# Kernel tuning notes

Hardware: AMD Instinct MI355X
Metric: run time of the kernel (lower is better)

Reference implementation:

```python
import jax, jax.numpy as jnp
import numpy as np

B, N, D, H, FF = 2, 2048, 768, 12, 3072
HD = D // H
RADIUS = 2.0
COORD_DIM = 3
LN_EPS = 1e-5


def _layernorm(x, g, b):
    m = jnp.mean(x, axis=-1, keepdims=True)
    v = jnp.mean((x - m) ** 2, axis=-1, keepdims=True)
    return (x - m) * jax.lax.rsqrt(v + LN_EPS) * g + b


def setup_inputs() -> dict:
    key = jax.random.key(0)
    ks = jax.random.split(key, 16)
    s = 0.02
    return {
        "x": jax.random.normal(ks[0], (B, N, D), jnp.float32),
        "coords": jax.random.uniform(ks[1], (B, N, COORD_DIM), jnp.float32) * 10.0,
        "w_qkv": jax.random.normal(ks[2], (D, 3 * D), jnp.float32) * s,
        "b_qkv": jnp.zeros((3 * D,), jnp.float32),
        "w_out": jax.random.normal(ks[3], (D, D), jnp.float32) * s,
        "b_out": jnp.zeros((D,), jnp.float32),
        "w_ff1": jax.random.normal(ks[4], (D, FF), jnp.float32) * s,
        "b_ff1": jnp.zeros((FF,), jnp.float32),
        "w_ff2": jax.random.normal(ks[5], (FF, D), jnp.float32) * s,
        "b_ff2": jnp.zeros((D,), jnp.float32),
        "g1": jnp.ones((D,), jnp.float32),
        "beta1": jnp.zeros((D,), jnp.float32),
        "g2": jnp.ones((D,), jnp.float32),
        "beta2": jnp.zeros((D,), jnp.float32),
    }


def reference(x, coords, w_qkv, b_qkv, w_out, b_out, w_ff1, b_ff1,
              w_ff2, b_ff2, g1, beta1, g2, beta2):
    # --- attention sub-block ---
    residual = x
    xn = _layernorm(x, g1, beta1)
    qkv = xn @ w_qkv + b_qkv                       # [B,N,3D]
    qkv = qkv.reshape(B, N, 3, H, HD)
    q, k, v = qkv[:, :, 0], qkv[:, :, 1], qkv[:, :, 2]   # [B,N,H,HD]

    # geometric radius mask: attend only to tokens within Euclidean RADIUS
    d2 = jnp.sum((coords[:, :, None, :] - coords[:, None, :, :]) ** 2, axis=-1)  # [B,N,N]
    mask = d2 <= RADIUS * RADIUS                   # self-distance 0 -> always true

    scores = jnp.einsum("bqhd,bkhd->bhqk", q, k) / jnp.sqrt(jnp.float32(HD))
    scores = jnp.where(mask[:, None, :, :], scores, jnp.float32(-1e9))
    attn = jax.nn.softmax(scores, axis=-1)
    attn_out = jnp.einsum("bhqk,bkhd->bqhd", attn, v).reshape(B, N, D)
    attn_out = attn_out @ w_out + b_out            # dropout=0 (eval)
    x = residual + attn_out

    # --- FFN sub-block ---
    residual = x
    xn = _layernorm(x, g2, beta2)
    h = jax.nn.gelu(xn @ w_ff1 + b_ff1, approximate=False)
    ff_out = h @ w_ff2 + b_ff2
    return residual + ff_out
```

## Files before the change

kernel.cpp:

```cpp
#include <hip/hip_runtime.h>
#include <hip/hip_bf16.h>

typedef unsigned short ushort_t;
typedef __attribute__((ext_vector_type(4))) float f32x4;
typedef __attribute__((ext_vector_type(8))) short s16x8;

#define DEV static __device__ __forceinline__

constexpr int Bb = 2, Nn = 2048, Dd = 768, Hh = 12, FFf = 3072;
constexpr int MTOK = Bb * Nn;
constexpr int QKVN = 3 * Dd;

DEV unsigned short f2bf(float f) {
    union { float f; unsigned int i; } x; x.f = f;
    unsigned int r = x.i + 0x7FFFu + ((x.i >> 16) & 1u);
    return (unsigned short)(r >> 16);
}

DEV void gload16(const void* g, void* l) {
    __builtin_amdgcn_global_load_lds(
        (const __attribute__((address_space(1))) void*)g,
        (__attribute__((address_space(3))) void*)l, 16, 0, 0);
}

DEV int xcd_swz(int lin, int n) {
    return (lin & 7) * (n >> 3) + (lin >> 3);
}

DEV float gelu_fast(float x) {
    float u = x * (0.7978845608f + 0.0356774081f * x * x);
    float e = __builtin_amdgcn_exp2f(2.885390082f * u);
    float th = 1.f - 2.f / (e + 1.f);
    return 0.5f * x * (1.f + th);
}

__global__ void k_transpose_all(const float* __restrict__ w_qkv, const float* __restrict__ w_out,
                                const float* __restrict__ w_ff1, const float* __restrict__ w_ff2,
                                unsigned short* __restrict__ o_qkv, unsigned short* __restrict__ o_out,
                                unsigned short* __restrict__ o_ff1, unsigned short* __restrict__ o_ff2) {
    __shared__ float t[32][33];
    int id = blockIdx.x;
    const float* in; unsigned short* out; int K, N, tid;
    if (id < 1728)      { in = w_qkv; out = o_qkv; K = 768;  N = 2304; tid = id; }
    else if (id < 2304) { in = w_out; out = o_out; K = 768;  N = 768;  tid = id - 1728; }
    else if (id < 4608) { in = w_ff1; out = o_ff1; K = 768;  N = 3072; tid = id - 2304; }
    else                { in = w_ff2; out = o_ff2; K = 3072; N = 768;  tid = id - 4608; }
    int nbx = N >> 5;
    int bx = (tid % nbx) * 32, by = (tid / nbx) * 32;
    int tx = threadIdx.x, ty = threadIdx.y;
#pragma unroll
    for (int i = 0; i < 4; i++)
        t[ty + 8 * i][tx] = in[(size_t)(by + ty + 8 * i) * N + bx + tx];
    __syncthreads();
#pragma unroll
    for (int i = 0; i < 4; i++)
        out[(size_t)(bx + ty + 8 * i) * K + by + tx] = f2bf(t[tx][ty + 8 * i]);
}

DEV int cell3(float x, float y, float z) {
    int cx = (int)(x * 0.5f); cx = cx > 4 ? 4 : cx;
    int cy = (int)(y * 0.5f); cy = cy > 4 ? 4 : cy;
    int cz = (int)(z * 0.5f); cz = cz > 4 ? 4 : cz;
    return (cz * 5 + cy) * 5 + cx;
}

__global__ __launch_bounds__(256) void k_sort(const float* __restrict__ coords,
                                              int* __restrict__ s2o,
                                              float4* __restrict__ c4s) {
    int b = blockIdx.y;
    int i = blockIdx.x * 4 + (threadIdx.x >> 6);
    int lane = threadIdx.x & 63;
    const float* cb = coords + (size_t)b * Nn * 3;
    float cix = cb[3 * i], ciy = cb[3 * i + 1], ciz = cb[3 * i + 2];
    int celli = cell3(cix, ciy, ciz);
    int pos = 0;
    for (int it = 0; it < Nn / 64; it++) {
        int j = it * 64 + lane;
        int cj = cell3(cb[3 * j], cb[3 * j + 1], cb[3 * j + 2]);
        bool before = (cj < celli) || (cj == celli && j < i);
        pos += __popcll(__ballot(before));
    }
    if (lane == 0) {
        s2o[b * Nn + pos] = i;
        c4s[b * Nn + pos] = make_float4(cix, ciy, ciz, 0.f);
    }
}

__global__ __launch_bounds__(256) void k_mask(const float4* __restrict__ c4s,
                                              unsigned long long* __restrict__ mb) {
    int qt = blockIdx.x, ks = blockIdx.y, b = blockIdx.z;
    __shared__ float4 ck[256];
    int t = threadIdx.x;
    ck[t] = c4s[b * Nn + ks * 256 + t];
    __syncthreads();
    int r = t >> 2, c = t & 3;
    int q = qt * 64 + r;
    float4 cq = c4s[b * Nn + q];
    unsigned long long w = 0;
#pragma unroll 8
    for (int j = 0; j < 64; j++) {
        float4 k4 = ck[c * 64 + j];
        float dx = __fsub_rn(cq.x, k4.x);
        float dy = __fsub_rn(cq.y, k4.y);
        float dz = __fsub_rn(cq.z, k4.z);
        float d2 = __fadd_rn(__fadd_rn(__fmul_rn(dx, dx), __fmul_rn(dy, dy)),
                             __fmul_rn(dz, dz));
        if (d2 <= 4.0f) w |= 1ull << j;
    }
    mb[((size_t)(b * Nn + q) << 5) + ks * 4 + c] = w;
}

__global__ __launch_bounds__(64) void k_tiles(const unsigned long long* __restrict__ mb,
                                              int* __restrict__ tl) {
    int q64 = blockIdx.x, b = blockIdx.y;
    int lane = threadIdx.x;
    unsigned long long v = 0;
    if (lane < 32) {
        const unsigned long long* base = mb + ((size_t)(b * Nn + q64 * 64) << 5) + lane;
        for (int r = 0; r < 64; r++) v |= base[(size_t)r << 5];
    }
    unsigned long long nz = __ballot(v != 0);
    int idx = __popcll(nz & ((1ull << lane) - 1));
    int* o = tl + (b * 32 + q64) * 33;
    if (v != 0) o[1 + idx] = lane;
    if (lane == 0) o[0] = __popcll(nz);
}

__global__ __launch_bounds__(128) void k_gatherK(const unsigned short* __restrict__ qkv,
                                                 const int* __restrict__ s2o,
                                                 unsigned short* __restrict__ Ksort) {
    int ns = blockIdx.x & (Nn - 1);
    int b = blockIdx.x >> 11;
    int t = threadIdx.x;
    int orig = s2o[b * Nn + ns];
    const s16x8* src = (const s16x8*)(qkv + ((size_t)b * Nn + orig) * QKVN + Dd);
    s16x8* dst = (s16x8*)(Ksort + ((size_t)b * Nn + ns) * Dd);
    if (t < 96) dst[t] = src[t];
}

__global__ __launch_bounds__(256) void k_vt(const unsigned short* __restrict__ qkv,
                                            const int* __restrict__ s2o,
                                            unsigned short* __restrict__ VtT) {
    __shared__ unsigned short Ld[64][72];
    int ns0 = blockIdx.x * 64;
    int bh = blockIdx.y;
    int b = bh / Hh, h = bh % Hh;
    int t = threadIdx.x;
#pragma unroll
    for (int i = 0; i < 2; i++) {
        int item = t + 256 * i;
        int row = item >> 3, ch = (item & 7) * 8;
        int orig = s2o[b * Nn + ns0 + row];
        *(s16x8*)&Ld[row][ch] =
            *(const s16x8*)(qkv + ((size_t)b * Nn + orig) * QKVN + 2 * Dd + h * 64 + ch);
    }
    __syncthreads();
    int vd = (t >> 5) * 8, vkp = (t & 31) * 2;
#pragma unroll
    for (int j = 0; j < 8; j++) {
        unsigned int pack = (unsigned int)Ld[vkp][vd + j] |
                            ((unsigned int)Ld[vkp + 1][vd + j] << 16);
        *(unsigned int*)((char*)VtT +
                         (((size_t)bh * 64 + vd + j) * Nn + ns0 + vkp) * 2) = pack;
    }
}

DEV float wred_sum(float v) {
#pragma unroll
    for (int o = 32; o; o >>= 1) v += __shfl_down(v, o, 64);
    return v;
}

__global__ __launch_bounds__(256) void k_ln(const float* __restrict__ x,
                                            const float* __restrict__ g,
                                            const float* __restrict__ be,
                                            unsigned short* __restrict__ out) {
    int row = blockIdx.x;
    const float* xr = x + (size_t)row * Dd;
    int t = threadIdx.x;
    float v0 = xr[t], v1 = xr[t + 256], v2 = xr[t + 512];
    float s = v0 + v1 + v2;
    float sq = v0 * v0 + v1 * v1 + v2 * v2;
    __shared__ float r1[4], r2[4];
    float ws = wred_sum(s), wq = wred_sum(sq);
    int wid = t >> 6, lane = t & 63;
    if (lane == 0) { r1[wid] = ws; r2[wid] = wq; }
    __syncthreads();
    s = r1[0] + r1[1] + r1[2] + r1[3];
    sq = r2[0] + r2[1] + r2[2] + r2[3];
    float mean = s * (1.f / Dd);
    float var = sq * (1.f / Dd) - mean * mean;
    float rs = rsqrtf(var + 1e-5f);
    unsigned short* orow = out + (size_t)row * Dd;
    orow[t]       = f2bf((v0 - mean) * rs * g[t]       + be[t]);
    orow[t + 256] = f2bf((v1 - mean) * rs * g[t + 256] + be[t + 256]);
    orow[t + 512] = f2bf((v2 - mean) * rs * g[t + 512] + be[t + 512]);
}

template <int EPI>
__global__ __launch_bounds__(512, 2) void k_gemm256(const unsigned short* __restrict__ A,
                                                    const unsigned short* __restrict__ Bt,
                                                    const float* __restrict__ bias,
                                                    unsigned short* __restrict__ outp,
                                                    int M, int N, int K) {
    constexpr int BM = 256, BN = 256, BK = 32;
    __shared__ unsigned short As[3][BM * BK];
    __shared__ unsigned short Bs[3][BN * BK];
    int NB = N >> 8;
    int id = xcd_swz(blockIdx.x, gridDim.x);
    int m0 = (id / NB) * BM, n0 = (id % NB) * BN;
    int t = threadIdx.x;
    int wid = t >> 6, lane = t & 63;
    int wr = wid >> 2, wc = wid & 3;
    int lg = lane >> 4, lr = lane & 15;
    f32x4 acc[8][4] = {};

    int srow = t >> 2, sch = t & 3;
    auto stage = [&](int buf, int kt) {
        int k0 = kt * BK;
#pragma unroll
        for (int g = 0; g < 2; g++) {
            int ar = g * 128 + srow;
            gload16(A + (size_t)(m0 + ar) * K + k0 + ((sch ^ (ar & 3)) * 8),
                    (char*)As[buf] + g * 8192 + wid * 1024);
        }
#pragma unroll
        for (int g = 0; g < 2; g++) {
            int br = g * 128 + srow;
            gload16(Bt + (size_t)(n0 + br) * K + k0 + ((sch ^ (br & 3)) * 8),
                    (char*)Bs[buf] + g * 8192 + wid * 1024);
        }
    };

    int NT = K / BK;
    stage(0, 0);
    stage(1, 1);
    for (int k = 0; k < NT; k++) {
        int cur = k % 3;
        if (k + 1 < NT) {
            asm volatile("s_waitcnt vmcnt(4)" ::: "memory");
        } else {
            asm volatile("s_waitcnt vmcnt(0)" ::: "memory");
        }
        __builtin_amdgcn_sched_barrier(0);
        __builtin_amdgcn_s_barrier();
        __builtin_amdgcn_sched_barrier(0);
        if (k + 2 < NT) stage((k + 2) % 3, k + 2);
        s16x8 af[8], bfr[4];
#pragma unroll
        for (int i = 0; i < 8; i++) {
            int row = wr * 128 + i * 16 + lr;
            af[i] = *(const s16x8*)((const char*)As[cur] + row * 64 + ((lg ^ (row & 3)) << 4));
        }
#pragma unroll
        for (int j = 0; j < 4; j++) {
            int row = wc * 64 + j * 16 + lr;
            bfr[j] = *(const s16x8*)((const char*)Bs[cur] + row * 64 + ((lg ^ (row & 3)) << 4));
        }
#pragma unroll
        for (int i = 0; i < 8; i++)
#pragma unroll
            for (int j = 0; j < 4; j++)
                acc[i][j] = __builtin_amdgcn_mfma_f32_16x16x32_bf16(
                    af[i], bfr[j], acc[i][j], 0, 0, 0);
    }

    int mrow = m0 + wr * 128;
    int ncol = n0 + wc * 64;
#pragma unroll
    for (int i = 0; i < 8; i++) {
#pragma unroll
        for (int j = 0; j < 4; j++) {
            int nn = ncol + j * 16 + lr;
            float bs = bias[nn];
#pragma unroll
            for (int r = 0; r < 4; r++) {
                int mm = mrow + i * 16 + lg * 4 + r;
                float v = acc[i][j][r] + bs;
                if (EPI == 1) v = gelu_fast(v);
                outp[(size_t)mm * N + nn] = f2bf(v);
            }
        }
    }
}

#define GEMM_PIPE_LOOP(NT)                                                              \
    stage(0, 0);                                                                        \
    if ((NT) > 1) stage(1, 1);                                                          \
    for (int t = 0; t < (NT); t++) {                                                    \
        int cur = t % 3;                                                                \
        if (t + 2 < (NT)) {                                                             \
            stage((t + 2) % 3, t + 2);                                                  \
            asm volatile("s_waitcnt vmcnt(8)" ::: "memory");                            \
        } else if (t + 1 < (NT)) {                                                      \
            asm volatile("s_waitcnt vmcnt(4)" ::: "memory");                            \
        } else {                                                                        \
            asm volatile("s_waitcnt vmcnt(0)" ::: "memory");                            \
        }                                                                               \
        __builtin_amdgcn_sched_barrier(0);                                              \
        __builtin_amdgcn_s_barrier();                                                   \
        const unsigned short* Ab = As[cur];                                             \
        const unsigned short* Bbp = Bs[cur];                                            \
        s16x8 af[4], bfr[4];                                                            \
        _Pragma("unroll")                                                               \
        for (int i = 0; i < 4; i++) {                                                   \
            af[i]  = *(const s16x8*)&Ab[(wr * 64 + i * 16 + lr) * 32 + lg * 8];         \
            bfr[i] = *(const s16x8*)&Bbp[(wc * 64 + i * 16 + lr) * 32 + lg * 8];        \
        }                                                                               \
        _Pragma("unroll")                                                               \
        for (int mi = 0; mi < 4; mi++)                                                  \
            _Pragma("unroll")                                                           \
            for (int ni = 0; ni < 4; ni++)                                              \
                acc[mi][ni] = __builtin_amdgcn_mfma_f32_16x16x32_bf16(                  \
                    af[mi], bfr[ni], acc[mi][ni], 0, 0, 0);                             \
        __builtin_amdgcn_s_barrier();                                                   \
    }

template <int SPLIT>
__global__ __launch_bounds__(256) void k_gemm_sk(const unsigned short* __restrict__ A,
                                                 const unsigned short* __restrict__ Bt,
                                                 float* __restrict__ part,
                                                 int M, int N, int K) {
    constexpr int BM = 128, BN = 128, BK = 32;
    __shared__ unsigned short As[3][BM * BK];
    __shared__ unsigned short Bs[3][BN * BK];
    int NB = N >> 7, MB = M >> 7;
    int id = xcd_swz(blockIdx.x, gridDim.x);
    int nb = id % NB;
    int mbk = (id / NB) % MB;
    int kz = id / (NB * MB);
    int m0 = mbk * BM, n0 = nb * BN;
    int Kc = K / SPLIT, kb = kz * (Kc / BK);
    int t = threadIdx.x;
    int wid = t >> 6, lane = t & 63;
    int wr = wid >> 1, wc = wid & 1;
    int lg = lane >> 4, lr = lane & 15;
    f32x4 acc[4][4] = {};

    int srow = wid * 32 + (lane >> 2);
    int scol = (lane & 3) * 8;
    const unsigned short* Ag = A + (size_t)(m0 + srow) * K + scol;
    const unsigned short* Bg = Bt + (size_t)(n0 + srow) * K + scol;

    auto stage = [&](int buf, int kt) {
        int k0 = (kb + kt) * BK;
        char* Al = (char*)As[buf] + wid * 2048;
        char* Bl = (char*)Bs[buf] + wid * 2048;
        gload16(Ag + k0, Al);
        gload16(Ag + k0 + (size_t)16 * K, Al + 1024);
        gload16(Bg + k0, Bl);
        gload16(Bg + k0 + (size_t)16 * K, Bl + 1024);
    };
    int nt = Kc / BK;
    GEMM_PIPE_LOOP(nt)

    float* po = part + (size_t)kz * M * N;
    int mrow = m0 + wr * 64;
    int ncol = n0 + wc * 64;
#pragma unroll
    for (int mi = 0; mi < 4; mi++)
#pragma unroll
        for (int ni = 0; ni < 4; ni++) {
            int nn = ncol + ni * 16 + lr;
#pragma unroll
            for (int r = 0; r < 4; r++) {
                int mm = mrow + mi * 16 + lg * 4 + r;
                po[(size_t)mm * N + nn] = acc[mi][ni][r];
            }
        }
}

__global__ __launch_bounds__(256) void k_reduce4_ln(const float* __restrict__ part,
                                                    const float* __restrict__ bias,
                                                    const float* __restrict__ res,
                                                    const float* __restrict__ g,
                                                    const float* __restrict__ be,
                                                    float* __restrict__ x2,
                                                    unsigned short* __restrict__ xn,
                                                    int MN) {
    int wid = threadIdx.x >> 6, lane = threadIdx.x & 63;
    int row = blockIdx.x * 4 + wid;
    size_t base = (size_t)row * Dd;
    f32x4 v[3];
    float s = 0.f, sq = 0.f;
#pragma unroll
    for (int j = 0; j < 3; j++) {
        int col = j * 256 + lane * 4;
        f32x4 a0 = *(const f32x4*)(part + base + col);
        f32x4 a1 = *(const f32x4*)(part + (size_t)MN + base + col);
        f32x4 a2 = *(const f32x4*)(part + 2 * (size_t)MN + base + col);
        f32x4 a3 = *(const f32x4*)(part + 3 * (size_t)MN + base + col);
        f32x4 r = *(const f32x4*)(res + base + col);
        f32x4 bs = *(const f32x4*)(bias + col);
#pragma unroll
        for (int q = 0; q < 4; q++) {
            v[j][q] = (a0[q] + a1[q]) + (a2[q] + a3[q]) + bs[q] + r[q];
            s += v[j][q];
            sq += v[j][q] * v[j][q];
        }
        *(f32x4*)(x2 + base + col) = v[j];
    }
    s = wred_sum(s); sq = wred_sum(sq);
    s = __shfl(s, 0, 64); sq = __shfl(sq, 0, 64);
    float mean = s * (1.f / Dd);
    float var = sq * (1.f / Dd) - mean * mean;
    float rs = rsqrtf(var + 1e-5f);
#pragma unroll
    for (int j = 0; j < 3; j++) {
        int col = j * 256 + lane * 4;
        f32x4 gg = *(const f32x4*)(g + col);
        f32x4 bb = *(const f32x4*)(be + col);
        ushort4 o;
        o.x = f2bf((v[j][0] - mean) * rs * gg[0] + bb[0]);
        o.y = f2bf((v[j][1] - mean) * rs * gg[1] + bb[1]);
        o.z = f2bf((v[j][2] - mean) * rs * gg[2] + bb[2]);
        o.w = f2bf((v[j][3] - mean) * rs * gg[3] + bb[3]);
        *(ushort4*)(xn + base + col) = o;
    }
}

__global__ __launch_bounds__(256) void k_reduce4(const float* __restrict__ part,
                                                 const float* __restrict__ bias,
                                                 const float* __restrict__ res,
                                                 float* __restrict__ out,
                                                 int MN, int N) {
    int i = (blockIdx.x * 256 + threadIdx.x) * 4;
    f32x4 a0 = *(const f32x4*)(part + i);
    f32x4 a1 = *(const f32x4*)(part + (size_t)MN + i);
    f32x4 a2 = *(const f32x4*)(part + 2 * (size_t)MN + i);
    f32x4 a3 = *(const f32x4*)(part + 3 * (size_t)MN + i);
    f32x4 r = *(const f32x4*)(res + i);
    f32x4 bs = *(const f32x4*)(bias + (i % N));
    f32x4 o;
#pragma unroll
    for (int j = 0; j < 4; j++) o[j] = (a0[j] + a1[j]) + (a2[j] + a3[j]) + bs[j] + r[j];
    *(f32x4*)(out + i) = o;
}

constexpr float SC2 = 0.125f * 1.44269504088896340736f;
constexpr float PMASK = -3.0e38f;
constexpr float MINIT = -1.0e30f;

__global__ __launch_bounds__(256) void k_attn(const unsigned short* __restrict__ qkv,
                                              const unsigned short* __restrict__ Ksort,
                                              const unsigned short* __restrict__ VtT,
                                              const int* __restrict__ s2o,
                                              const uint2* __restrict__ mb,
                                              const int* __restrict__ tl,
                                              unsigned short* __restrict__ out) {
    int lin = blockIdx.x;
    int id = (lin & 7) * 96 + (lin >> 3);
    int q64 = id & 31;
    int hb = id >> 5;
    int h = hb % Hh, b = hb / Hh;
    int bh = b * Hh + h;

    __shared__ __align__(16) char sm[2 * 16384 + 4 * 2048];

    int t = threadIdx.x, wid = t >> 6, lane = t & 63;
    int lg = lane >> 4, lr = lane & 15;
    int sw = lr & 7;
    int qbase = q64 * 64 + wid * 16;

    int oq = s2o[b * Nn + qbase + lr];
    const unsigned short* Qb = qkv + ((size_t)b * Nn + oq) * QKVN + h * 64;
    s16x8 qf0 = *(const s16x8*)(Qb + lg * 8);
    s16x8 qf1 = *(const s16x8*)(Qb + 32 + lg * 8);

    const uint2* mrow = mb + ((size_t)(b * Nn + qbase + lr) << 5);
    const int* tle = tl + (b * 32 + q64) * 33;
    int tlv = (lane < 33) ? tle[lane] : 0;
    int cnt = __shfl(tlv, 0, 64);

    int srow = lane >> 3, sch = lane & 7;
    int krow = wid * 8 + srow;
    int kx = sch ^ (krow & 7);
    const unsigned short* Kg0 = Ksort + ((size_t)b * Nn + krow) * Dd + h * 64 + kx * 8;
    const unsigned short* Vg0 = VtT + ((size_t)bh * 64 + krow) * Nn + kx * 8;
    char* pw = sm + 32768 + wid * 2048 + lr * 128;

    float m2 = MINIT, l_run = 0.f;
    f32x4 oacc[4] = {};

    int tid0 = __shfl(tlv, 1, 64);
    uint2 Mw = mrow[tid0];
    {
        char* Kl = sm + wid * 1024;
        gload16(Kg0 + (size_t)(tid0 * 64) * Dd, Kl);
        gload16(Kg0 + (size_t)(tid0 * 64 + 32) * Dd, Kl + 4096);
        char* Vl = sm + 8192 + wid * 1024;
        gload16(Vg0 + tid0 * 64, Vl);
        gload16(Vg0 + tid0 * 64 + 32 * (size_t)Nn, Vl + 4096);
    }
    __syncthreads();

    for (int ti = 0; ti < cnt; ti++) {
        int cur = ti & 1;
        uint2 MwN;
        if (ti + 1 < cnt) {
            int tidn = __shfl(tlv, 2 + ti, 64);
            char* Kl = sm + (cur ^ 1) * 16384 + wid * 1024;
            gload16(Kg0 + (size_t)(tidn * 64) * Dd, Kl);
            gload16(Kg0 + (size_t)(tidn * 64 + 32) * Dd, Kl + 4096);
            char* Vl = sm + (cur ^ 1) * 16384 + 8192 + wid * 1024;
            gload16(Vg0 + tidn * 64, Vl);
            gload16(Vg0 + tidn * 64 + 32 * (size_t)Nn, Vl + 4096);
            MwN = mrow[tidn];
        }

        if (__any((Mw.x | Mw.y) != 0)) {
            const char* Kbuf = sm + cur * 16384;
            const char* Vbuf = Kbuf + 8192;

            __builtin_amdgcn_s_setprio(1);
            f32x4 st[4];
#pragma unroll
            for (int s = 0; s < 4; s++) {
                const char* kr = Kbuf + (s * 16 + lr) * 128;
                s16x8 kf0 = *(const s16x8*)(kr + ((lg ^ sw) << 4));
                s16x8 kf1 = *(const s16x8*)(kr + (((4 + lg) ^ sw) << 4));
                f32x4 z = {};
                z = __builtin_amdgcn_mfma_f32_16x16x32_bf16(kf0, qf0, z, 0, 0, 0);
                st[s] = __builtin_amdgcn_mfma_f32_16x16x32_bf16(kf1, qf1, z, 0, 0, 0);
            }
            __builtin_amdgcn_s_setprio(0);

            float p[4][4];
            float mt = PMASK;
#pragma unroll
            for (int s = 0; s < 4; s++) {
                unsigned int wsel = (s < 2) ? Mw.x : Mw.y;
#pragma unroll
                for (int r = 0; r < 4; r++) {
                    float sv = st[s][r] * SC2;
                    unsigned int bit = (wsel >> ((s & 1) * 16 + lg * 4 + r)) & 1u;
                    p[s][r] = bit ? sv : PMASK;
                    mt = fmaxf(mt, p[s][r]);
                }
            }
            mt = fmaxf(mt, __shfl_xor(mt, 16, 64));
            mt = fmaxf(mt, __shfl_xor(mt, 32, 64));

            if (!__all(mt <= m2 + 11.5416f)) {
                float mn2 = fmaxf(m2, mt);
                float fac = __builtin_amdgcn_exp2f(m2 - mn2);
                l_run *= fac;
                m2 = mn2;
                float fr[4];
#pragma unroll
                for (int r = 0; r < 4; r++) fr[r] = __shfl(fac, (lane & 48) + lg * 4 + r, 64);
#pragma unroll
                for (int dt = 0; dt < 4; dt++)
#pragma unroll
                    for (int r = 0; r < 4; r++) oacc[dt][r] *= fr[r];
            }

            float lt = 0.f;
#pragma unroll
            for (int s = 0; s < 4; s++)
#pragma unroll
                for (int r = 0; r < 4; r++) {
                    p[s][r] = __builtin_amdgcn_exp2f(p[s][r] - m2);
                    lt += p[s][r];
                }
            lt += __shfl_xor(lt, 16, 64);
            lt += __shfl_xor(lt, 32, 64);
            l_run += lt;

#pragma unroll
            for (int s = 0; s < 4; s++) {
                unsigned int lo = (unsigned int)f2bf(p[s][0]) | ((unsigned int)f2bf(p[s][1]) << 16);
                unsigned int hi = (unsigned int)f2bf(p[s][2]) | ((unsigned int)f2bf(p[s][3]) << 16);
                unsigned long long u = (unsigned long long)lo | ((unsigned long long)hi << 32);
                int chunk = (s * 2 + (lg >> 1)) ^ sw;
                *(unsigned long long*)(pw + (chunk << 4) + (lg & 1) * 8) = u;
            }

            __builtin_amdgcn_s_setprio(1);
#pragma unroll
            for (int c = 0; c < 2; c++) {
                s16x8 pf = *(const s16x8*)(pw + (((c * 4 + lg) ^ sw) << 4));
#pragma unroll
                for (int dt = 0; dt < 4; dt++) {
                    const char* vr = Vbuf + (dt * 16 + lr) * 128;
                    s16x8 vf = *(const s16x8*)(vr + (((c * 4 + lg) ^ sw) << 4));
                    oacc[dt] = __builtin_amdgcn_mfma_f32_16x16x32_bf16(pf, vf, oacc[dt], 0, 0, 0);
                }
            }
            __builtin_amdgcn_s_setprio(0);
        }

        __syncthreads();
        Mw = MwN;
    }

    float lr4[4];
    int orow[4];
#pragma unroll
    for (int r = 0; r < 4; r++) {
        lr4[r] = __shfl(l_run, (lane & 48) + lg * 4 + r, 64);
        orow[r] = s2o[b * Nn + qbase + lg * 4 + r];
    }
#pragma unroll
    for (int dt = 0; dt < 4; dt++)
#pragma unroll
        for (int r = 0; r < 4; r++) {
            float v = oacc[dt][r] / lr4[r];
            out[((size_t)b * Nn + orow[r]) * Dd + h * 64 + dt * 16 + lr] = f2bf(v);
        }
}

extern "C" void kernel_launch(void* const* d_in, const int* in_sizes, int n_in,
                              void* d_out, int out_size, void* d_ws, size_t ws_size,
                              hipStream_t stream) {
    const float* x      = (const float*)d_in[0];
    const float* coords = (const float*)d_in[1];
    const float* w_qkv  = (const float*)d_in[2];
    const float* b_qkv  = (const float*)d_in[3];
    const float* w_out  = (const float*)d_in[4];
    const float* b_out  = (const float*)d_in[5];
    const float* w_ff1  = (const float*)d_in[6];
    const float* b_ff1  = (const float*)d_in[7];
    const float* w_ff2  = (const float*)d_in[8];
    const float* b_ff2  = (const float*)d_in[9];
    const float* g1     = (const float*)d_in[10];
    const float* beta1  = (const float*)d_in[11];
    const float* g2     = (const float*)d_in[12];
    const float* beta2  = (const float*)d_in[13];

    char* ws = (char*)d_ws;
    size_t off = 0;
    auto alloc = [&](size_t bytes) {
        char* p = ws + off;
        off += (bytes + 255) & ~(size_t)255;
        return p;
    };
    unsigned short* w_qkv_t = (unsigned short*)alloc((size_t)QKVN * Dd * 2);
    unsigned short* w_out_t = (unsigned short*)alloc((size_t)Dd * Dd * 2);
    unsigned short* w_ff1_t = (unsigned short*)alloc((size_t)FFf * Dd * 2);
    unsigned short* w_ff2_t = (unsigned short*)alloc((size_t)Dd * FFf * 2);
    float4*         c4s     = (float4*)alloc((size_t)MTOK * 16);
    int*            s2o     = (int*)alloc((size_t)MTOK * 4);
    unsigned long long* mbits = (unsigned long long*)alloc((size_t)MTOK * 32 * 8);
    int*            tl      = (int*)alloc((size_t)Bb * 32 * 33 * 4);
    unsigned short* xn      = (unsigned short*)alloc((size_t)MTOK * Dd * 2);
    unsigned short* hbuf    = (unsigned short*)alloc((size_t)MTOK * FFf * 2);
    float*          x2      = (float*)alloc((size_t)MTOK * Dd * 4);
    unsigned short* attn_o  = (unsigned short*)alloc((size_t)MTOK * Dd * 2);
    unsigned short* qkv     = (unsigned short*)alloc((size_t)MTOK * QKVN * 2);
    unsigned short* Ksort   = (unsigned short*)alloc((size_t)MTOK * Dd * 2);
    unsigned short* VtT     = (unsigned short*)alloc((size_t)Bb * Hh * 64 * Nn * 2);
    float*          partial = (float*)alloc((size_t)4 * MTOK * Dd * 4);

    k_transpose_all<<<dim3(6912), dim3(32, 8), 0, stream>>>(
        w_qkv, w_out, w_ff1, w_ff2, w_qkv_t, w_out_t, w_ff1_t, w_ff2_t);
    k_sort<<<dim3(Nn / 4, Bb), 256, 0, stream>>>(coords, s2o, c4s);
    k_mask<<<dim3(Nn / 64, 8, Bb), 256, 0, stream>>>(c4s, mbits);
    k_tiles<<<dim3(32, Bb), 64, 0, stream>>>(mbits, tl);

    k_ln<<<MTOK, 256, 0, stream>>>(x, g1, beta1, xn);
    k_gemm256<0><<<dim3((MTOK / 256) * (QKVN / 256)), 512, 0, stream>>>(
        xn, w_qkv_t, b_qkv, qkv, MTOK, QKVN, Dd);
    k_gatherK<<<dim3(MTOK), 128, 0, stream>>>(qkv, s2o, Ksort);
    k_vt<<<dim3(Nn / 64, Bb * Hh), 256, 0, stream>>>(qkv, s2o, VtT);
    k_attn<<<dim3((Nn / 64) * Hh * Bb), 256, 0, stream>>>(
        qkv, Ksort, VtT, s2o, (const uint2*)mbits, tl, attn_o);
    k_gemm_sk<4><<<dim3((Dd / 128) * (MTOK / 128) * 4), 256, 0, stream>>>(
        attn_o, w_out_t, partial, MTOK, Dd, Dd);
    k_reduce4_ln<<<dim3(MTOK / 4), 256, 0, stream>>>(
        partial, b_out, x, g2, beta2, x2, xn, MTOK * Dd);
    k_gemm256<1><<<dim3((MTOK / 256) * (FFf / 256)), 512, 0, stream>>>(
        xn, w_ff1_t, b_ff1, hbuf, MTOK, FFf, Dd);
    k_gemm_sk<4><<<dim3((Dd / 128) * (MTOK / 128) * 4), 256, 0, stream>>>(
        hbuf, w_ff2_t, partial, MTOK, Dd, FFf);
    k_reduce4<<<dim3(MTOK * Dd / 1024), 256, 0, stream>>>(
        partial, b_ff2, x2, (float*)d_out, MTOK * Dd, Dd);
}
```

Before: 226.6 us.

## Run the whole block in spatially sorted token order and swap the GEMM tile

The first layernorm now gathers tokens into sorted order, so QKV, attention, the projections and the FFN all run on sorted rows. The final reduce scatters results back to the original positions. This removes the separate K gather kernel, the Ksort buffer and the indirect loads in k_vt and k_attn. The 256x256 BK32 triple-buffered GEMM for QKV and FF1 is also replaced by a 128x128 BK64 double-buffered kernel, which gives more blocks but less reuse per block.

```diff
diff --git a/kernel.cpp b/kernel.cpp
--- a/kernel.cpp
+++ b/kernel.cpp
@@ -126,20 +126,7 @@
     if (lane == 0) o[0] = __popcll(nz);
 }
 
-__global__ __launch_bounds__(128) void k_gatherK(const unsigned short* __restrict__ qkv,
-                                                 const int* __restrict__ s2o,
-                                                 unsigned short* __restrict__ Ksort) {
-    int ns = blockIdx.x & (Nn - 1);
-    int b = blockIdx.x >> 11;
-    int t = threadIdx.x;
-    int orig = s2o[b * Nn + ns];
-    const s16x8* src = (const s16x8*)(qkv + ((size_t)b * Nn + orig) * QKVN + Dd);
-    s16x8* dst = (s16x8*)(Ksort + ((size_t)b * Nn + ns) * Dd);
-    if (t < 96) dst[t] = src[t];
-}
-
 __global__ __launch_bounds__(256) void k_vt(const unsigned short* __restrict__ qkv,
-                                            const int* __restrict__ s2o,
                                             unsigned short* __restrict__ VtT) {
     __shared__ unsigned short Ld[64][72];
     int ns0 = blockIdx.x * 64;
@@ -150,9 +137,8 @@
     for (int i = 0; i < 2; i++) {
         int item = t + 256 * i;
         int row = item >> 3, ch = (item & 7) * 8;
-        int orig = s2o[b * Nn + ns0 + row];
         *(s16x8*)&Ld[row][ch] =
-            *(const s16x8*)(qkv + ((size_t)b * Nn + orig) * QKVN + 2 * Dd + h * 64 + ch);
+            *(const s16x8*)(qkv + ((size_t)b * Nn + ns0 + row) * QKVN + 2 * Dd + h * 64 + ch);
     }
     __syncthreads();
     int vd = (t >> 5) * 8, vkp = (t & 31) * 2;
@@ -171,12 +157,14 @@
     return v;
 }
 
-__global__ __launch_bounds__(256) void k_ln(const float* __restrict__ x,
-                                            const float* __restrict__ g,
-                                            const float* __restrict__ be,
-                                            unsigned short* __restrict__ out) {
+__global__ __launch_bounds__(256) void k_ln_g(const float* __restrict__ x,
+                                              const int* __restrict__ s2o,
+                                              const float* __restrict__ g,
+                                              const float* __restrict__ be,
+                                              unsigned short* __restrict__ out) {
     int row = blockIdx.x;
-    const float* xr = x + (size_t)row * Dd;
+    int orig = (row & ~(Nn - 1)) | s2o[row];
+    const float* xr = x + (size_t)orig * Dd;
     int t = threadIdx.x;
     float v0 = xr[t], v1 = xr[t + 256], v2 = xr[t + 512];
     float s = v0 + v1 + v2;
@@ -198,123 +186,98 @@
 }
 
 template <int EPI>
-__global__ __launch_bounds__(512, 2) void k_gemm256(const unsigned short* __restrict__ A,
-                                                    const unsigned short* __restrict__ Bt,
-                                                    const float* __restrict__ bias,
-                                                    unsigned short* __restrict__ outp,
-                                                    int M, int N, int K) {
-    constexpr int BM = 256, BN = 256, BK = 32;
-    __shared__ unsigned short As[3][BM * BK];
-    __shared__ unsigned short Bs[3][BN * BK];
-    int NB = N >> 8;
+__global__ __launch_bounds__(256) void k_gemm64(const unsigned short* __restrict__ A,
+                                                const unsigned short* __restrict__ Bt,
+                                                const float* __restrict__ bias,
+                                                unsigned short* __restrict__ outp,
+                                                int M, int N, int K) {
+    constexpr int BM = 128, BN = 128, BK = 64;
+    __shared__ unsigned short As[2][BM * BK];
+    __shared__ unsigned short Bs[2][BN * BK];
+    int NB = N >> 7;
     int id = xcd_swz(blockIdx.x, gridDim.x);
     int m0 = (id / NB) * BM, n0 = (id % NB) * BN;
     int t = threadIdx.x;
     int wid = t >> 6, lane = t & 63;
-    int wr = wid >> 2, wc = wid & 3;
+    int wr = wid >> 1, wc = wid & 1;
     int lg = lane >> 4, lr = lane & 15;
-    f32x4 acc[8][4] = {};
-
-    int srow = t >> 2, sch = t & 3;
+    int sw = lr & 7;
+    f32x4 acc[4][4] = {};
+
+    int srow = lane >> 3;
+    int sch = (lane & 7) ^ srow;
+    const unsigned short* Ag = A + (size_t)m0 * K + sch * 8;
+    const unsigned short* Bg = Bt + (size_t)n0 * K + sch * 8;
+
     auto stage = [&](int buf, int kt) {
         int k0 = kt * BK;
 #pragma unroll
-        for (int g = 0; g < 2; g++) {
-            int ar = g * 128 + srow;
-            gload16(A + (size_t)(m0 + ar) * K + k0 + ((sch ^ (ar & 3)) * 8),
-                    (char*)As[buf] + g * 8192 + wid * 1024);
-        }
-#pragma unroll
-        for (int g = 0; g < 2; g++) {
-            int br = g * 128 + srow;
-            gload16(Bt + (size_t)(n0 + br) * K + k0 + ((sch ^ (br & 3)) * 8),
-                    (char*)Bs[buf] + g * 8192 + wid * 1024);
+        for (int g = 0; g < 4; g++) {
+            int row = wid * 32 + g * 8 + srow;
+            gload16(Ag + (size_t)row * K + k0, (char*)As[buf] + (wid * 4 + g) * 1024);
+        }
+#pragma unroll
+        for (int g = 0; g < 4; g++) {
+            int row = wid * 32 + g * 8 + srow;
+            gload16(Bg + (size_t)row * K + k0, (char*)Bs[buf] + (wid * 4 + g) * 1024);
         }
     };
 
     int NT = K / BK;
     stage(0, 0);
-    stage(1, 1);
     for (int k = 0; k < NT; k++) {
-        int cur = k % 3;
+        int cur = k & 1;
         if (k + 1 < NT) {
-            asm volatile("s_waitcnt vmcnt(4)" ::: "memory");
+            stage(cur ^ 1, k + 1);
+            asm volatile("s_waitcnt vmcnt(8)" ::: "memory");
         } else {
             asm volatile("s_waitcnt vmcnt(0)" ::: "memory");
         }
         __builtin_amdgcn_sched_barrier(0);
         __builtin_amdgcn_s_barrier();
-        __builtin_amdgcn_sched_barrier(0);
-        if (k + 2 < NT) stage((k + 2) % 3, k + 2);
-        s16x8 af[8], bfr[4];
-#pragma unroll
-        for (int i = 0; i < 8; i++) {
-            int row = wr * 128 + i * 16 + lr;
-            af[i] = *(const s16x8*)((const char*)As[cur] + row * 64 + ((lg ^ (row & 3)) << 4));
-        }
-#pragma unroll
-        for (int j = 0; j < 4; j++) {
-            int row = wc * 64 + j * 16 + lr;
-            bfr[j] = *(const s16x8*)((const char*)Bs[cur] + row * 64 + ((lg ^ (row & 3)) << 4));
-        }
-#pragma unroll
-        for (int i = 0; i < 8; i++)
-#pragma unroll
-            for (int j = 0; j < 4; j++)
-                acc[i][j] = __builtin_amdgcn_mfma_f32_16x16x32_bf16(
-                    af[i], bfr[j], acc[i][j], 0, 0, 0);
-    }
-
-    int mrow = m0 + wr * 128;
+        const char* Ab = (const char*)As[cur];
+        const char* Bbp = (const char*)Bs[cur];
+#pragma unroll
+        for (int s = 0; s < 2; s++) {
+            s16x8 af[4], bfr[4];
+#pragma unroll
+            for (int i = 0; i < 4; i++) {
+                int row = wr * 64 + i * 16 + lr;
+                af[i] = *(const s16x8*)(Ab + row * 128 + (((s * 4 + lg) ^ sw) << 4));
+            }
+#pragma unroll
+            for (int j = 0; j < 4; j++) {
+                int row = wc * 64 + j * 16 + lr;
+                bfr[j] = *(const s16x8*)(Bbp + row * 128 + (((s * 4 + lg) ^ sw) << 4));
+            }
+#pragma unroll
+            for (int mi = 0; mi < 4; mi++)
+#pragma unroll
+                for (int ni = 0; ni < 4; ni++)
+                    acc[mi][ni] = __builtin_amdgcn_mfma_f32_16x16x32_bf16(
+                        af[mi], bfr[ni], acc[mi][ni], 0, 0, 0);
+        }
+        __builtin_amdgcn_s_barrier();
+    }
+
+    int mrow = m0 + wr * 64;
     int ncol = n0 + wc * 64;
 #pragma unroll
-    for (int i = 0; i < 8; i++) {
-#pragma unroll
-        for (int j = 0; j < 4; j++) {
-            int nn = ncol + j * 16 + lr;
+    for (int mi = 0; mi < 4; mi++) {
+#pragma unroll
+        for (int ni = 0; ni < 4; ni++) {
+            int nn = ncol + ni * 16 + lr;
             float bs = bias[nn];
 #pragma unroll
             for (int r = 0; r < 4; r++) {
-                int mm = mrow + i * 16 + lg * 4 + r;
-                float v = acc[i][j][r] + bs;
+                int mm = mrow + mi * 16 + lg * 4 + r;
+                float v = acc[mi][ni][r] + bs;
                 if (EPI == 1) v = gelu_fast(v);
                 outp[(size_t)mm * N + nn] = f2bf(v);
             }
         }
     }
 }
-
-#define GEMM_PIPE_LOOP(NT)                                                              \
-    stage(0, 0);                                                                        \
-    if ((NT) > 1) stage(1, 1);                                                          \
-    for (int t = 0; t < (NT); t++) {                                                    \
-        int cur = t % 3;                                                                \
-        if (t + 2 < (NT)) {                                                             \
-            stage((t + 2) % 3, t + 2);                                                  \
-            asm volatile("s_waitcnt vmcnt(8)" ::: "memory");                            \
-        } else if (t + 1 < (NT)) {                                                      \
-            asm volatile("s_waitcnt vmcnt(4)" ::: "memory");                            \
-        } else {                                                                        \
-            asm volatile("s_waitcnt vmcnt(0)" ::: "memory");                            \
-        }                                                                               \
-        __builtin_amdgcn_sched_barrier(0);                                              \
-        __builtin_amdgcn_s_barrier();                                                   \
-        const unsigned short* Ab = As[cur];                                             \
-        const unsigned short* Bbp = Bs[cur];                                            \
-        s16x8 af[4], bfr[4];                                                            \
-        _Pragma("unroll")                                                               \
-        for (int i = 0; i < 4; i++) {                                                   \
-            af[i]  = *(const s16x8*)&Ab[(wr * 64 + i * 16 + lr) * 32 + lg * 8];         \
-            bfr[i] = *(const s16x8*)&Bbp[(wc * 64 + i * 16 + lr) * 32 + lg * 8];        \
-        }                                                                               \
-        _Pragma("unroll")                                                               \
-        for (int mi = 0; mi < 4; mi++)                                                  \
-            _Pragma("unroll")                                                           \
-            for (int ni = 0; ni < 4; ni++)                                              \
-                acc[mi][ni] = __builtin_amdgcn_mfma_f32_16x16x32_bf16(                  \
-                    af[mi], bfr[ni], acc[mi][ni], 0, 0, 0);                             \
-        __builtin_amdgcn_s_barrier();                                                   \
-    }
 
 template <int SPLIT>
 __global__ __launch_bounds__(256) void k_gemm_sk(const unsigned short* __restrict__ A,
@@ -352,7 +315,36 @@
         gload16(Bg + k0 + (size_t)16 * K, Bl + 1024);
     };
     int nt = Kc / BK;
-    GEMM_PIPE_LOOP(nt)
+    stage(0, 0);
+    if (nt > 1) stage(1, 1);
+    for (int k = 0; k < nt; k++) {
+        int cur = k % 3;
+        if (k + 2 < nt) {
+            stage((k + 2) % 3, k + 2);
+            asm volatile("s_waitcnt vmcnt(8)" ::: "memory");
+        } else if (k + 1 < nt) {
+            asm volatile("s_waitcnt vmcnt(4)" ::: "memory");
+        } else {
+            asm volatile("s_waitcnt vmcnt(0)" ::: "memory");
+        }
+        __builtin_amdgcn_sched_barrier(0);
+        __builtin_amdgcn_s_barrier();
+        const unsigned short* Ab = As[cur];
+        const unsigned short* Bbp = Bs[cur];
+        s16x8 af[4], bfr[4];
+#pragma unroll
+        for (int i = 0; i < 4; i++) {
+            af[i]  = *(const s16x8*)&Ab[(wr * 64 + i * 16 + lr) * 32 + lg * 8];
+            bfr[i] = *(const s16x8*)&Bbp[(wc * 64 + i * 16 + lr) * 32 + lg * 8];
+        }
+#pragma unroll
+        for (int mi = 0; mi < 4; mi++)
+#pragma unroll
+            for (int ni = 0; ni < 4; ni++)
+                acc[mi][ni] = __builtin_amdgcn_mfma_f32_16x16x32_bf16(
+                    af[mi], bfr[ni], acc[mi][ni], 0, 0, 0);
+        __builtin_amdgcn_s_barrier();
+    }
 
     float* po = part + (size_t)kz * M * N;
     int mrow = m0 + wr * 64;
@@ -372,7 +364,8 @@
 
 __global__ __launch_bounds__(256) void k_reduce4_ln(const float* __restrict__ part,
                                                     const float* __restrict__ bias,
-                                                    const float* __restrict__ res,
+                                                    const float* __restrict__ x,
+                                                    const int* __restrict__ s2o,
                                                     const float* __restrict__ g,
                                                     const float* __restrict__ be,
                                                     float* __restrict__ x2,
@@ -380,7 +373,9 @@
                                                     int MN) {
     int wid = threadIdx.x >> 6, lane = threadIdx.x & 63;
     int row = blockIdx.x * 4 + wid;
+    int orig = (row & ~(Nn - 1)) | s2o[row];
     size_t base = (size_t)row * Dd;
+    size_t obase = (size_t)orig * Dd;
     f32x4 v[3];
     float s = 0.f, sq = 0.f;
 #pragma unroll
@@ -390,7 +385,7 @@
         f32x4 a1 = *(const f32x4*)(part + (size_t)MN + base + col);
         f32x4 a2 = *(const f32x4*)(part + 2 * (size_t)MN + base + col);
         f32x4 a3 = *(const f32x4*)(part + 3 * (size_t)MN + base + col);
-        f32x4 r = *(const f32x4*)(res + base + col);
+        f32x4 r = *(const f32x4*)(x + obase + col);
         f32x4 bs = *(const f32x4*)(bias + col);
 #pragma unroll
         for (int q = 0; q < 4; q++) {
@@ -419,22 +414,32 @@
     }
 }
 
-__global__ __launch_bounds__(256) void k_reduce4(const float* __restrict__ part,
-                                                 const float* __restrict__ bias,
-                                                 const float* __restrict__ res,
-                                                 float* __restrict__ out,
-                                                 int MN, int N) {
-    int i = (blockIdx.x * 256 + threadIdx.x) * 4;
-    f32x4 a0 = *(const f32x4*)(part + i);
-    f32x4 a1 = *(const f32x4*)(part + (size_t)MN + i);
-    f32x4 a2 = *(const f32x4*)(part + 2 * (size_t)MN + i);
-    f32x4 a3 = *(const f32x4*)(part + 3 * (size_t)MN + i);
-    f32x4 r = *(const f32x4*)(res + i);
-    f32x4 bs = *(const f32x4*)(bias + (i % N));
-    f32x4 o;
-#pragma unroll
-    for (int j = 0; j < 4; j++) o[j] = (a0[j] + a1[j]) + (a2[j] + a3[j]) + bs[j] + r[j];
-    *(f32x4*)(out + i) = o;
+__global__ __launch_bounds__(256) void k_reduce4_sc(const float* __restrict__ part,
+                                                    const float* __restrict__ bias,
+                                                    const float* __restrict__ res,
+                                                    const int* __restrict__ s2o,
+                                                    float* __restrict__ out,
+                                                    int MN) {
+    int wid = threadIdx.x >> 6, lane = threadIdx.x & 63;
+    int row = blockIdx.x * 4 + wid;
+    int orig = (row & ~(Nn - 1)) | s2o[row];
+    size_t base = (size_t)row * Dd;
+    size_t obase = (size_t)orig * Dd;
+#pragma unroll
+    for (int j = 0; j < 3; j++) {
+        int col = j * 256 + lane * 4;
+        f32x4 a0 = *(const f32x4*)(part + base + col);
+        f32x4 a1 = *(const f32x4*)(part + (size_t)MN + base + col);
+        f32x4 a2 = *(const f32x4*)(part + 2 * (size_t)MN + base + col);
+        f32x4 a3 = *(const f32x4*)(part + 3 * (size_t)MN + base + col);
+        f32x4 r = *(const f32x4*)(res + base + col);
+        f32x4 bs = *(const f32x4*)(bias + col);
+        f32x4 o;
+#pragma unroll
+        for (int q = 0; q < 4; q++)
+            o[q] = (a0[q] + a1[q]) + (a2[q] + a3[q]) + bs[q] + r[q];
+        *(f32x4*)(out + obase + col) = o;
+    }
 }
 
 constexpr float SC2 = 0.125f * 1.44269504088896340736f;
@@ -442,9 +447,7 @@
 constexpr float MINIT = -1.0e30f;
 
 __global__ __launch_bounds__(256) void k_attn(const unsigned short* __restrict__ qkv,
-                                              const unsigned short* __restrict__ Ksort,
                                               const unsigned short* __restrict__ VtT,
-                                              const int* __restrict__ s2o,
                                               const uint2* __restrict__ mb,
                                               const int* __restrict__ tl,
                                               unsigned short* __restrict__ out) {
@@ -462,8 +465,7 @@
     int sw = lr & 7;
     int qbase = q64 * 64 + wid * 16;
 
-    int oq = s2o[b * Nn + qbase + lr];
-    const unsigned short* Qb = qkv + ((size_t)b * Nn + oq) * QKVN + h * 64;
+    const unsigned short* Qb = qkv + ((size_t)b * Nn + qbase + lr) * QKVN + h * 64;
     s16x8 qf0 = *(const s16x8*)(Qb + lg * 8);
     s16x8 qf1 = *(const s16x8*)(Qb + 32 + lg * 8);
 
@@ -475,7 +477,7 @@
     int srow = lane >> 3, sch = lane & 7;
     int krow = wid * 8 + srow;
     int kx = sch ^ (krow & 7);
-    const unsigned short* Kg0 = Ksort + ((size_t)b * Nn + krow) * Dd + h * 64 + kx * 8;
+    const unsigned short* Kg0 = qkv + ((size_t)b * Nn + krow) * QKVN + Dd + h * 64 + kx * 8;
     const unsigned short* Vg0 = VtT + ((size_t)bh * 64 + krow) * Nn + kx * 8;
     char* pw = sm + 32768 + wid * 2048 + lr * 128;
 
@@ -486,8 +488,8 @@
     uint2 Mw = mrow[tid0];
     {
         char* Kl = sm + wid * 1024;
-        gload16(Kg0 + (size_t)(tid0 * 64) * Dd, Kl);
-        gload16(Kg0 + (size_t)(tid0 * 64 + 32) * Dd, Kl + 4096);
+        gload16(Kg0 + (size_t)(tid0 * 64) * QKVN, Kl);
+        gload16(Kg0 + (size_t)(tid0 * 64 + 32) * QKVN, Kl + 4096);
         char* Vl = sm + 8192 + wid * 1024;
         gload16(Vg0 + tid0 * 64, Vl);
         gload16(Vg0 + tid0 * 64 + 32 * (size_t)Nn, Vl + 4096);
@@ -500,8 +502,8 @@
         if (ti + 1 < cnt) {
             int tidn = __shfl(tlv, 2 + ti, 64);
             char* Kl = sm + (cur ^ 1) * 16384 + wid * 1024;
-            gload16(Kg0 + (size_t)(tidn * 64) * Dd, Kl);
-            gload16(Kg0 + (size_t)(tidn * 64 + 32) * Dd, Kl + 4096);
+            gload16(Kg0 + (size_t)(tidn * 64) * QKVN, Kl);
+            gload16(Kg0 + (size_t)(tidn * 64 + 32) * QKVN, Kl + 4096);
             char* Vl = sm + (cur ^ 1) * 16384 + 8192 + wid * 1024;
             gload16(Vg0 + tidn * 64, Vl);
             gload16(Vg0 + tidn * 64 + 32 * (size_t)Nn, Vl + 4096);
@@ -595,18 +597,15 @@
     }
 
     float lr4[4];
-    int orow[4];
-#pragma unroll
-    for (int r = 0; r < 4; r++) {
+#pragma unroll
+    for (int r = 0; r < 4; r++)
         lr4[r] = __shfl(l_run, (lane & 48) + lg * 4 + r, 64);
-        orow[r] = s2o[b * Nn + qbase + lg * 4 + r];
-    }
 #pragma unroll
     for (int dt = 0; dt < 4; dt++)
 #pragma unroll
         for (int r = 0; r < 4; r++) {
             float v = oacc[dt][r] / lr4[r];
-            out[((size_t)b * Nn + orow[r]) * Dd + h * 64 + dt * 16 + lr] = f2bf(v);
+            out[((size_t)b * Nn + qbase + lg * 4 + r) * Dd + h * 64 + dt * 16 + lr] = f2bf(v);
         }
 }
 
@@ -648,7 +647,6 @@
     float*          x2      = (float*)alloc((size_t)MTOK * Dd * 4);
     unsigned short* attn_o  = (unsigned short*)alloc((size_t)MTOK * Dd * 2);
     unsigned short* qkv     = (unsigned short*)alloc((size_t)MTOK * QKVN * 2);
-    unsigned short* Ksort   = (unsigned short*)alloc((size_t)MTOK * Dd * 2);
     unsigned short* VtT     = (unsigned short*)alloc((size_t)Bb * Hh * 64 * Nn * 2);
     float*          partial = (float*)alloc((size_t)4 * MTOK * Dd * 4);
 
@@ -658,21 +656,20 @@
     k_mask<<<dim3(Nn / 64, 8, Bb), 256, 0, stream>>>(c4s, mbits);
     k_tiles<<<dim3(32, Bb), 64, 0, stream>>>(mbits, tl);
 
-    k_ln<<<MTOK, 256, 0, stream>>>(x, g1, beta1, xn);
-    k_gemm256<0><<<dim3((MTOK / 256) * (QKVN / 256)), 512, 0, stream>>>(
+    k_ln_g<<<MTOK, 256, 0, stream>>>(x, s2o, g1, beta1, xn);
+    k_gemm64<0><<<dim3((QKVN / 128) * (MTOK / 128)), 256, 0, stream>>>(
         xn, w_qkv_t, b_qkv, qkv, MTOK, QKVN, Dd);
-    k_gatherK<<<dim3(MTOK), 128, 0, stream>>>(qkv, s2o, Ksort);
-    k_vt<<<dim3(Nn / 64, Bb * Hh), 256, 0, stream>>>(qkv, s2o, VtT);
+    k_vt<<<dim3(Nn / 64, Bb * Hh), 256, 0, stream>>>(qkv, VtT);
     k_attn<<<dim3((Nn / 64) * Hh * Bb), 256, 0, stream>>>(
-        qkv, Ksort, VtT, s2o, (const uint2*)mbits, tl, attn_o);
+        qkv, VtT, (const uint2*)mbits, tl, attn_o);
     k_gemm_sk<4><<<dim3((Dd / 128) * (MTOK / 128) * 4), 256, 0, stream>>>(
         attn_o, w_out_t, partial, MTOK, Dd, Dd);
     k_reduce4_ln<<<dim3(MTOK / 4), 256, 0, stream>>>(
-        partial, b_out, x, g2, beta2, x2, xn, MTOK * Dd);
-    k_gemm256<1><<<dim3((MTOK / 256) * (FFf / 256)), 512, 0, stream>>>(
+        partial, b_out, x, s2o, g2, beta2, x2, xn, MTOK * Dd);
+    k_gemm64<1><<<dim3((FFf / 128) * (MTOK / 128)), 256, 0, stream>>>(
         xn, w_ff1_t, b_ff1, hbuf, MTOK, FFf, Dd);
     k_gemm_sk<4><<<dim3((Dd / 128) * (MTOK / 128) * 4), 256, 0, stream>>>(
         hbuf, w_ff2_t, partial, MTOK, Dd, FFf);
-    k_reduce4<<<dim3(MTOK * Dd / 1024), 256, 0, stream>>>(
-        partial, b_ff2, x2, (float*)d_out, MTOK * Dd, Dd);
-}
+    k_reduce4_sc<<<dim3(MTOK / 4), 256, 0, stream>>>(
+        partial, b_ff2, x2, s2o, (float*)d_out, MTOK * Dd);
+}
```

Measured after the change: 207.2 us. -8.6%, faster.
